# Kernel optimization log

Hardware: AMD Instinct MI355X
Metric: run time of the kernel (lower is better)

The kernel has to match this reference:

```python
import math
import jax, jax.numpy as jnp
import numpy as np

D = 256       # d_model
R = 64        # low-rank bottleneck
E = 3         # num experts
KS = (1, 3, 5)
EPS = 0.1     # sinkhorn epsilon
ITERS = 10    # sinkhorn iterations


def _ln(x, g, b):
    m = jnp.mean(x, -1, keepdims=True)
    v = jnp.mean((x - m) ** 2, -1, keepdims=True)
    return (x - m) * jax.lax.rsqrt(v + 1e-5) * g + b


def _gelu(x):
    return jax.nn.gelu(x, approximate=False)  # torch nn.GELU default (erf)


def setup_inputs() -> dict:
    key = jax.random.key(0)
    ks = jax.random.split(key, 12)
    s = 0.02
    B, Lt, La = 16, 1024, 2048
    return {
        "text_feat": jax.random.normal(ks[0], (B, Lt, D), jnp.float32),
        "audio_feat": jax.random.normal(ks[1], (B, La, D), jnp.float32),
        # shared OT projection (LayerNorm + Linear, shared across modalities)
        "ln_g": jnp.ones((D,), jnp.float32),
        "ln_b": jnp.zeros((D,), jnp.float32),
        "W_sh": jax.random.normal(ks[2], (D, D), jnp.float32) * s,
        "b_sh": jnp.zeros((D,), jnp.float32),
        # contradiction router: Linear(d+1->d) GELU Linear(d->E)
        "Wr1": jax.random.normal(ks[3], (D, D + 1), jnp.float32) * s,
        "br1": jnp.zeros((D,), jnp.float32),
        "Wr2": jax.random.normal(ks[4], (E, D), jnp.float32) * s,
        "br2": jnp.zeros((E,), jnp.float32),
        # 3 low-rank conv experts (stacked where shapes match)
        "down_W": jax.random.normal(ks[5], (E, R, D), jnp.float32) * s,
        "down_b": jnp.zeros((E, R), jnp.float32),
        "conv_w1": jax.random.normal(ks[6], (R, R, 1), jnp.float32) * s,
        "conv_w3": jax.random.normal(ks[7], (R, R, 3), jnp.float32) * s,
        "conv_w5": jax.random.normal(ks[8], (R, R, 5), jnp.float32) * s,
        "conv_b": jnp.zeros((E, R), jnp.float32),
        "up_W": jax.random.normal(ks[9], (E, D, R), jnp.float32) * s,
        "up_b": jnp.zeros((E, D), jnp.float32),
        "en_g": jnp.ones((E, D), jnp.float32),
        "en_b": jnp.zeros((E, D), jnp.float32),
    }


def reference(text_feat, audio_feat, ln_g, ln_b, W_sh, b_sh, Wr1, br1, Wr2, br2,
              down_W, down_b, conv_w1, conv_w3, conv_w5, conv_b, up_W, up_b, en_g, en_b):
    B, Lt, _ = text_feat.shape
    La = audio_feat.shape[1]

    # ---- shared projection (dropout = identity at eval) ----
    Tp = _ln(text_feat, ln_g, ln_b) @ W_sh.T + b_sh      # [B,Lt,D]
    Ap = _ln(audio_feat, ln_g, ln_b) @ W_sh.T + b_sh     # [B,La,D]

    # ---- cosine cost ----
    Tn = Tp / jnp.maximum(jnp.linalg.norm(Tp, axis=-1, keepdims=True), 1e-12)
    An = Ap / jnp.maximum(jnp.linalg.norm(Ap, axis=-1, keepdims=True), 1e-12)
    cost = 1.0 - jnp.einsum('bmd,bnd->bmn', Tn, An)      # [B,Lt,La]

    # ---- log-domain Sinkhorn (uniform marginals, no masks) ----
    log_K = -cost / (EPS + 1e-8)
    log_mu = jnp.full((B, Lt), -math.log(Lt), jnp.float32)
    log_nu = jnp.full((B, La), -math.log(La), jnp.float32)
    lu = jnp.zeros((B, Lt), jnp.float32)
    lv = jnp.zeros((B, La), jnp.float32)
    for _ in range(ITERS):
        lu = log_mu - jax.scipy.special.logsumexp(log_K + lv[:, None, :], axis=-1)
        lu = jnp.nan_to_num(jnp.clip(lu, -1e9, 1e9), nan=0.0, posinf=1e9, neginf=-1e9)
        lv = log_nu - jax.scipy.special.logsumexp(log_K + lu[:, :, None], axis=1)
        lv = jnp.nan_to_num(jnp.clip(lv, -1e9, 1e9), nan=0.0, posinf=1e9, neginf=-1e9)
    pi = jnp.exp(lu[:, :, None] + log_K + lv[:, None, :])
    pi = jnp.nan_to_num(pi, nan=0.0, posinf=1.0, neginf=0.0)  # [B,Lt,La]

    A_al = jnp.einsum('bmn,bnd->bmd', pi, Ap)            # [B,Lt,D]
    S = jnp.sum(Tp * A_al, -1)                           # [B,Lt]
    resid = jnp.abs(Tp - A_al)                           # [B,Lt,D]

    # ---- contradiction router ----
    rin = jnp.concatenate([S[..., None], resid], -1)     # [B,Lt,D+1]
    G = jax.nn.softmax(_gelu(rin @ Wr1.T + br1) @ Wr2.T + br2, axis=-1)  # [B,Lt,E]

    # ---- multi-scale low-rank conv MoE over contradiction residual ----
    convs = (conv_w1, conv_w3, conv_w5)
    x = resid
    out = jnp.zeros_like(Tp)
    for e in range(E):
        h = _gelu(x @ down_W[e].T + down_b[e])           # [B,Lt,R]
        k = convs[e].shape[-1]
        pad = (k - 1) // 2
        hc = jax.lax.conv_general_dilated(
            h.transpose(0, 2, 1), convs[e], (1,), [(pad, pad)],
            dimension_numbers=('NCH', 'OIH', 'NCH')) + conv_b[e][None, :, None]
        h = _gelu(hc).transpose(0, 2, 1)                 # [B,Lt,R]
        h = h @ up_W[e].T + up_b[e]                      # [B,Lt,D]
        eo = _ln(h + x, en_g[e], en_b[e])
        out = out + G[..., e:e + 1] * eo
    return out
```

## Files before the change

kernel.cpp:

```cpp
#include <hip/hip_runtime.h>
#include <cstdio>

#define D_ 256
#define LT 1024
#define LA 2048
#define NB 16
#define RR_ 64
#define NRT (NB*LT)
#define NRA (NB*LA)

#define DECQ  (-0.080645161f)
#define DECQ2 (-0.11634637f)

typedef short bf16x8 __attribute__((ext_vector_type(8)));
typedef float f32x4 __attribute__((ext_vector_type(4)));

__device__ __forceinline__ float gelu_f(float x) {
    return 0.5f * x * (1.0f + erff(x * 0.70710678118654752f));
}
__device__ __forceinline__ unsigned short f2bf(float f) {
    union { float f; unsigned int i; } c; c.f = f;
    unsigned int x = c.i;
    return (unsigned short)((x + 0x7fffu + ((x >> 16) & 1u)) >> 16);
}
__device__ __forceinline__ float exp2_fast(float x) {
#if __has_builtin(__builtin_amdgcn_exp2f)
    return __builtin_amdgcn_exp2f(x);
#else
    float r; asm("v_exp_f32 %0, %1" : "=v"(r) : "v"(x)); return r;
#endif
}
__device__ __forceinline__ unsigned int cvt_pk_bf16(float lo, float hi) {
    unsigned int r;
    asm("v_cvt_pk_bf16_f32 %0, %1, %2" : "=v"(r) : "v"(lo), "v"(hi));
    return r;
}

__global__ __launch_bounds__(256) void k_prep_all(
    const float* __restrict__ W_sh, const float* __restrict__ down_W,
    const float* __restrict__ up_W, const float* __restrict__ Wr1,
    unsigned short* __restrict__ Wb, unsigned short* __restrict__ dWb,
    unsigned short* __restrict__ uWb, unsigned short* __restrict__ Wr1b)
{
    int i = blockIdx.x * 256 + threadIdx.x;
    if (i < 65536) Wb[i] = f2bf(W_sh[i]);
    else if (i < 114688) { int j = i - 65536; dWb[j] = f2bf(down_W[j]); }
    else if (i < 163840) { int j = i - 114688; uWb[j] = f2bf(up_W[j]); }
    else { int j = i - 163840; int n = j >> 8, k = j & 255; Wr1b[j] = f2bf(Wr1[(long)n * 257 + 1 + k]); }
}

__global__ __launch_bounds__(256) void k_lnproj_mfma(
    const float* __restrict__ X, const float* __restrict__ g, const float* __restrict__ bln,
    const unsigned short* __restrict__ Wb, const float* __restrict__ bsh,
    float* __restrict__ Pf, unsigned short* __restrict__ Nb)
{
    __shared__ short xb[64][264];
    __shared__ short Bs[256][40];
    int tid = threadIdx.x;
    long row0 = (long)blockIdx.x * 64;
    {
        int lane = tid & 31, rg = tid >> 5;
        float4 ga = *(const float4*)(g + lane * 8);
        float4 gb2 = *(const float4*)(g + lane * 8 + 4);
        float4 ba = *(const float4*)(bln + lane * 8);
        float4 bb2 = *(const float4*)(bln + lane * 8 + 4);
        for (int it = 0; it < 8; it++) {
            int r = it * 8 + rg;
            const float4* xp4 = (const float4*)(X + (row0 + r) * D_);
            float4 a = xp4[lane * 2], b = xp4[lane * 2 + 1];
            float s = a.x + a.y + a.z + a.w + b.x + b.y + b.z + b.w;
#pragma unroll
            for (int off = 16; off >= 1; off >>= 1) s += __shfl_xor(s, off);
            float mean = s * (1.0f / 256.0f);
            float q = (a.x - mean) * (a.x - mean) + (a.y - mean) * (a.y - mean)
                    + (a.z - mean) * (a.z - mean) + (a.w - mean) * (a.w - mean)
                    + (b.x - mean) * (b.x - mean) + (b.y - mean) * (b.y - mean)
                    + (b.z - mean) * (b.z - mean) + (b.w - mean) * (b.w - mean);
#pragma unroll
            for (int off = 16; off >= 1; off >>= 1) q += __shfl_xor(q, off);
            float ivar = rsqrtf(q * (1.0f / 256.0f) + 1e-5f);
            unsigned int u0 = f2bf((a.x - mean) * ivar * ga.x + ba.x);
            unsigned int u1 = f2bf((a.y - mean) * ivar * ga.y + ba.y);
            unsigned int u2 = f2bf((a.z - mean) * ivar * ga.z + ba.z);
            unsigned int u3 = f2bf((a.w - mean) * ivar * ga.w + ba.w);
            unsigned int u4 = f2bf((b.x - mean) * ivar * gb2.x + bb2.x);
            unsigned int u5 = f2bf((b.y - mean) * ivar * gb2.y + bb2.y);
            unsigned int u6 = f2bf((b.z - mean) * ivar * gb2.z + bb2.z);
            unsigned int u7 = f2bf((b.w - mean) * ivar * gb2.w + bb2.w);
            int4 pv;
            pv.x = (int)(u0 | (u1 << 16)); pv.y = (int)(u2 | (u3 << 16));
            pv.z = (int)(u4 | (u5 << 16)); pv.w = (int)(u6 | (u7 << 16));
            *(int4*)&xb[r][lane * 8] = pv;
        }
    }
    __syncthreads();
    int wid = tid >> 6, lane = tid & 63;
    int l15 = lane & 15, kq = lane >> 4;
    int m_local = wid * 16;
    f32x4 acc[16];
#pragma unroll
    for (int j = 0; j < 16; j++) acc[j] = (f32x4){0.f, 0.f, 0.f, 0.f};
    for (int kt = 0; kt < 8; kt++) {
        int k0 = kt * 32;
#pragma unroll
        for (int h = 0; h < 4; h++) {
            int idx = tid + 256 * h;
            int n = idx >> 2, qc = idx & 3;
            *(int4*)&Bs[n][qc * 8] = *(const int4*)(Wb + (long)n * D_ + k0 + qc * 8);
        }
        __syncthreads();
        bf16x8 af = *(const bf16x8*)&xb[m_local + l15][k0 + kq * 8];
#pragma unroll
        for (int j = 0; j < 16; j++) {
            bf16x8 bf = *(const bf16x8*)&Bs[j * 16 + l15][kq * 8];
            acc[j] = __builtin_amdgcn_mfma_f32_16x16x32_bf16(af, bf, acc[j], 0, 0, 0);
        }
        __syncthreads();
    }
#pragma unroll
    for (int j = 0; j < 16; j++) {
        float bv = bsh[j * 16 + l15];
#pragma unroll
        for (int r = 0; r < 4; r++) acc[j][r] += bv;
    }
    float sq[4] = {0.f, 0.f, 0.f, 0.f};
#pragma unroll
    for (int j = 0; j < 16; j++)
#pragma unroll
        for (int r = 0; r < 4; r++) sq[r] += acc[j][r] * acc[j][r];
#pragma unroll
    for (int off = 8; off >= 1; off >>= 1) {
#pragma unroll
        for (int r = 0; r < 4; r++) sq[r] += __shfl_xor(sq[r], off);
    }
    float rinv[4];
#pragma unroll
    for (int r = 0; r < 4; r++) rinv[r] = 1.0f / fmaxf(sqrtf(sq[r]), 1e-12f);
#pragma unroll
    for (int j = 0; j < 16; j++) {
        int col = j * 16 + l15;
#pragma unroll
        for (int r = 0; r < 4; r++) {
            long m = row0 + m_local + kq * 4 + r;
            if (Pf) Pf[m * D_ + col] = acc[j][r];
            Nb[m * D_ + col] = f2bf(acc[j][r] * rinv[r]);
        }
    }
}

__global__ __launch_bounds__(256) void k_transpose_bf(
    const unsigned short* __restrict__ Anb, unsigned short* __restrict__ ApbT)
{
    __shared__ short t[64][68];
    int b = blockIdx.x;
    int n0 = blockIdx.y * 64;
    int d0 = blockIdx.z * 64;
    int tid = threadIdx.x;
#pragma unroll
    for (int h = 0; h < 2; h++) {
        int c = tid + 256 * h;
        int nr = c >> 3, ch = c & 7;
        *(int4*)&t[nr][ch * 8] = *(const int4*)(Anb + ((long)b * LA + n0 + nr) * D_ + d0 + ch * 8);
    }
    __syncthreads();
#pragma unroll
    for (int h = 0; h < 2; h++) {
        int c = tid + 256 * h;
        int d = c >> 3, nch = c & 7;
        unsigned short v[8];
#pragma unroll
        for (int k = 0; k < 8; k++) v[k] = (unsigned short)t[nch * 8 + k][d];
        int4 ov;
        ov.x = (int)((unsigned int)v[0] | ((unsigned int)v[1] << 16));
        ov.y = (int)((unsigned int)v[2] | ((unsigned int)v[3] << 16));
        ov.z = (int)((unsigned int)v[4] | ((unsigned int)v[5] << 16));
        ov.w = (int)((unsigned int)v[6] | ((unsigned int)v[7] << 16));
        *(int4*)(ApbT + ((long)b * D_ + d0 + d) * LA + n0 + nch * 8) = ov;
    }
}

__global__ __launch_bounds__(256) void k_cost_mfma(
    const unsigned short* __restrict__ Tnb, const unsigned short* __restrict__ Anb,
    unsigned char* __restrict__ logK8, unsigned char* __restrict__ logK8T)
{
    __shared__ short sm[2][128][48];
    short (*As)[48] = sm[0];
    short (*Bs)[48] = sm[1];
    unsigned char* tile = (unsigned char*)sm;
    int b = blockIdx.x;
    int m_blk = blockIdx.y * 128, n_blk = blockIdx.z * 128;
    int tid = threadIdx.x;
    int wid = tid >> 6, lane = tid & 63;
    int l15 = lane & 15, kq = lane >> 4;
    int wm0 = (wid >> 1) * 64, wn0 = (wid & 1) * 64;
    const unsigned short* Ab = Tnb + ((long)b * LT + m_blk) * D_;
    const unsigned short* Bb = Anb + ((long)b * LA + n_blk) * D_;
    f32x4 acc[4][4];
#pragma unroll
    for (int i = 0; i < 4; i++)
#pragma unroll
        for (int j = 0; j < 4; j++) acc[i][j] = (f32x4){0.f, 0.f, 0.f, 0.f};
    for (int kt = 0; kt < 8; kt++) {
        int k0 = kt * 32;
#pragma unroll
        for (int h = 0; h < 2; h++) {
            int idx = tid + 256 * h;
            int row = idx >> 2, ch = idx & 3;
            *(int4*)&As[row][ch * 8] = *(const int4*)(Ab + (long)row * D_ + k0 + ch * 8);
            *(int4*)&Bs[row][ch * 8] = *(const int4*)(Bb + (long)row * D_ + k0 + ch * 8);
        }
        __syncthreads();
        bf16x8 af[4], bfv[4];
#pragma unroll
        for (int i = 0; i < 4; i++) af[i] = *(const bf16x8*)&As[wm0 + i * 16 + l15][kq * 8];
#pragma unroll
        for (int j = 0; j < 4; j++) bfv[j] = *(const bf16x8*)&Bs[wn0 + j * 16 + l15][kq * 8];
#pragma unroll
        for (int i = 0; i < 4; i++)
#pragma unroll
            for (int j = 0; j < 4; j++)
                acc[i][j] = __builtin_amdgcn_mfma_f32_16x16x32_bf16(af[i], bfv[j], acc[i][j], 0, 0, 0);
        __syncthreads();
    }
#pragma unroll
    for (int i = 0; i < 4; i++) {
#pragma unroll
        for (int j = 0; j < 4; j++) {
            int n = wn0 + j * 16 + l15;
            long base = ((long)b * LT + m_blk + wm0 + i * 16 + kq * 4) * (long)LA + n_blk + n;
            unsigned int pk = 0;
#pragma unroll
            for (int r = 0; r < 4; r++) {
                float q = rintf((1.0f - acc[i][j][r]) * 124.0f);
                q = fminf(fmaxf(q, 0.0f), 255.0f);
                unsigned int qb = (unsigned int)q;
                pk |= qb << (8 * r);
                logK8[base + (long)r * LA] = (unsigned char)qb;
            }
            *(unsigned int*)&tile[n * 144 + wm0 + i * 16 + kq * 4] = pk;
        }
    }
    __syncthreads();
#pragma unroll
    for (int h = 0; h < 4; h++) {
        int idx = tid + 256 * h;
        int row = idx >> 3, ch = idx & 7;
        int4 v = *(const int4*)&tile[row * 144 + ch * 16];
        *(int4*)(logK8T + ((long)b * LA + n_blk + row) * (long)LT + m_blk + ch * 16) = v;
    }
}

__global__ __launch_bounds__(256) void k_rowlse2(
    const unsigned char* __restrict__ logK8, const float* __restrict__ lv2,
    float* __restrict__ lu2, int first)
{
    __shared__ float red[8][4];
    int b = blockIdx.x & 15;
    int mseg = blockIdx.x >> 4;
    int tid = threadIdx.x;
    int wid = tid >> 6, lane = tid & 63;
    float lvv[8] = {0.f, 0.f, 0.f, 0.f, 0.f, 0.f, 0.f, 0.f};
    if (!first) {
        const float* lvp = lv2 + (long)b * LA + tid * 8;
        float4 l0 = *(const float4*)lvp, l1 = *(const float4*)(lvp + 4);
        lvv[0] = l0.x; lvv[1] = l0.y; lvv[2] = l0.z; lvv[3] = l0.w;
        lvv[4] = l1.x; lvv[5] = l1.y; lvv[6] = l1.z; lvv[7] = l1.w;
    }
    const unsigned char* p = logK8 + ((long)b * LT + mseg * 8) * (long)LA + tid * 8;
#pragma unroll
    for (int r = 0; r < 8; r++) {
        uint2 w = *(const uint2*)(p + (long)r * LA);
        unsigned int w0 = w.x, w1 = w.y;
        float s = 0.f;
        s += exp2_fast(fmaf((float)(w0 & 0xffu),         DECQ2, lvv[0]));
        s += exp2_fast(fmaf((float)((w0 >> 8) & 0xffu),  DECQ2, lvv[1]));
        s += exp2_fast(fmaf((float)((w0 >> 16) & 0xffu), DECQ2, lvv[2]));
        s += exp2_fast(fmaf((float)(w0 >> 24),           DECQ2, lvv[3]));
        s += exp2_fast(fmaf((float)(w1 & 0xffu),         DECQ2, lvv[4]));
        s += exp2_fast(fmaf((float)((w1 >> 8) & 0xffu),  DECQ2, lvv[5]));
        s += exp2_fast(fmaf((float)((w1 >> 16) & 0xffu), DECQ2, lvv[6]));
        s += exp2_fast(fmaf((float)(w1 >> 24),           DECQ2, lvv[7]));
#pragma unroll
        for (int off = 32; off >= 1; off >>= 1) s += __shfl_xor(s, off);
        if (lane == 0) red[r][wid] = s;
    }
    __syncthreads();
    if (tid < 8) {
        float s = red[tid][0] + red[tid][1] + red[tid][2] + red[tid][3];
        lu2[(long)b * LT + mseg * 8 + tid] = -10.0f - __log2f(s);
    }
}

__global__ __launch_bounds__(256) void k_collse2(
    const unsigned char* __restrict__ logK8T, const float* __restrict__ lu2,
    float* __restrict__ lv2, int final_)
{
    __shared__ float red[16][2];
    int b = blockIdx.x & 15;
    int nseg = blockIdx.x >> 4;
    int tid = threadIdx.x;
    int t7 = tid & 127;
    int g = tid >> 7;
    int wid = tid >> 6, lane = tid & 63;
    const float* lup = lu2 + (long)b * LT + t7 * 8;
    float4 l0 = *(const float4*)lup, l1 = *(const float4*)(lup + 4);
    float lus[8] = {l0.x, l0.y, l0.z, l0.w, l1.x, l1.y, l1.z, l1.w};
    const unsigned char* base = logK8T + ((long)b * LA + nseg * 16) * (long)LT + t7 * 8;
#pragma unroll
    for (int it = 0; it < 8; it++) {
        int c = it * 2 + g;
        uint2 w = *(const uint2*)(base + (long)c * LT);
        unsigned int w0 = w.x, w1 = w.y;
        float s = 0.f;
        s += exp2_fast(fmaf((float)(w0 & 0xffu),         DECQ2, lus[0]));
        s += exp2_fast(fmaf((float)((w0 >> 8) & 0xffu),  DECQ2, lus[1]));
        s += exp2_fast(fmaf((float)((w0 >> 16) & 0xffu), DECQ2, lus[2]));
        s += exp2_fast(fmaf((float)(w0 >> 24),           DECQ2, lus[3]));
        s += exp2_fast(fmaf((float)(w1 & 0xffu),         DECQ2, lus[4]));
        s += exp2_fast(fmaf((float)((w1 >> 8) & 0xffu),  DECQ2, lus[5]));
        s += exp2_fast(fmaf((float)((w1 >> 16) & 0xffu), DECQ2, lus[6]));
        s += exp2_fast(fmaf((float)(w1 >> 24),           DECQ2, lus[7]));
#pragma unroll
        for (int off = 32; off >= 1; off >>= 1) s += __shfl_xor(s, off);
        if (lane == 0) red[c][wid & 1] = s;
    }
    __syncthreads();
    if (tid < 16) {
        float s = red[tid][0] + red[tid][1];
        lv2[(long)b * LA + nseg * 16 + tid] = final_ ? (0.00048828125f / s)
                                                     : (-11.0f - __log2f(s));
    }
}

__global__ __launch_bounds__(256) void k_scale_ev(
    unsigned short* __restrict__ ApbT, const float* __restrict__ ev)
{
    int b = blockIdx.x;
    int d = blockIdx.y;
    int tid = threadIdx.x;
    long off = ((long)b * D_ + d) * (long)LA + tid * 8;
    int4 v = *(const int4*)(ApbT + off);
    const float* ep = ev + (long)b * LA + tid * 8;
    float4 e0 = *(const float4*)ep, e1 = *(const float4*)(ep + 4);
    unsigned int u[4] = {(unsigned int)v.x, (unsigned int)v.y, (unsigned int)v.z, (unsigned int)v.w};
    float ee[8] = {e0.x, e0.y, e0.z, e0.w, e1.x, e1.y, e1.z, e1.w};
    unsigned int o[4];
#pragma unroll
    for (int k = 0; k < 4; k++) {
        float lo = __uint_as_float(u[k] << 16) * ee[2 * k];
        float hi = __uint_as_float(u[k] & 0xffff0000u) * ee[2 * k + 1];
        o[k] = cvt_pk_bf16(lo, hi);
    }
    int4 ov; ov.x = (int)o[0]; ov.y = (int)o[1]; ov.z = (int)o[2]; ov.w = (int)o[3];
    *(int4*)(ApbT + off) = ov;
}

__global__ __launch_bounds__(256) void k_pi2(
    const unsigned char* __restrict__ logK8, const unsigned short* __restrict__ Av,
    const float* __restrict__ lu2, float* __restrict__ Apart)
{
    __shared__ short As[32][48];
    __shared__ short Bs[256][48];
    __shared__ float eus[32];
    int b = blockIdx.x;
    int kh = blockIdx.y;
    int m_blk = blockIdx.z * 32;
    int nbase = kh * 1024;
    int tid = threadIdx.x;
    if (tid < 32) eus[tid] = exp2_fast(lu2[(long)b * LT + m_blk + tid]);
    int wid = tid >> 6, lane = tid & 63;
    int l15 = lane & 15, kq = lane >> 4;
    int wm0 = (wid & 1) * 16, wd0 = (wid >> 1) * 128;
    f32x4 acc[8];
#pragma unroll
    for (int j = 0; j < 8; j++) acc[j] = (f32x4){0.f, 0.f, 0.f, 0.f};
    const unsigned char* Kbase = logK8 + ((long)b * LT + m_blk) * (long)LA + nbase;
    const unsigned short* Bbase = Av + (long)b * D_ * (long)LA + nbase;
    int arow = tid >> 3, ac4 = (tid & 7) * 4;
    for (int kt = 0; kt < 32; kt++) {
        int n0 = kt * 32;
        {
            unsigned int w = *(const unsigned int*)(Kbase + (long)arow * LA + n0 + ac4);
            float e0 = exp2_fast((float)(w & 0xffu) * DECQ2);
            float e1 = exp2_fast((float)((w >> 8) & 0xffu) * DECQ2);
            float e2 = exp2_fast((float)((w >> 16) & 0xffu) * DECQ2);
            float e3 = exp2_fast((float)(w >> 24) * DECQ2);
            uint2 pv;
            pv.x = cvt_pk_bf16(e0, e1);
            pv.y = cvt_pk_bf16(e2, e3);
            *(uint2*)&As[arow][ac4] = pv;
        }
#pragma unroll
        for (int h = 0; h < 4; h++) {
            int idx = tid + 256 * h;
            int row = idx >> 2, ch = idx & 3;
            *(int4*)&Bs[row][ch * 8] = *(const int4*)(Bbase + (long)row * LA + n0 + ch * 8);
        }
        __syncthreads();
        bf16x8 af = *(const bf16x8*)&As[wm0 + l15][kq * 8];
        bf16x8 bfv[8];
#pragma unroll
        for (int j = 0; j < 8; j++) bfv[j] = *(const bf16x8*)&Bs[wd0 + j * 16 + l15][kq * 8];
#pragma unroll
        for (int j = 0; j < 8; j++)
            acc[j] = __builtin_amdgcn_mfma_f32_16x16x32_bf16(af, bfv[j], acc[j], 0, 0, 0);
        __syncthreads();
    }
    float* dst = Apart + (long)kh * (NB * (long)LT * D_);
#pragma unroll
    for (int r = 0; r < 4; r++) {
        int rloc = wm0 + kq * 4 + r;
        float eu = eus[rloc];
        long obase = ((long)b * LT + m_blk + rloc) * D_;
#pragma unroll
        for (int j = 0; j < 8; j++)
            dst[obase + wd0 + j * 16 + l15] = acc[j][r] * eu;
    }
}

__global__ __launch_bounds__(256) void k_sresid(
    const float* __restrict__ Tp, const float* __restrict__ Apart,
    float* __restrict__ resid, unsigned short* __restrict__ residb, float* __restrict__ S)
{
    __shared__ float red[4];
    int b = blockIdx.x & 15;
    int m = blockIdx.x >> 4;
    long row = (long)b * LT + m;
    int tid = threadIdx.x;
    long idx = row * D_ + tid;
    float t = Tp[idx];
    float a = Apart[idx] + Apart[idx + (long)NB * LT * D_];
    float rr = fabsf(t - a);
    resid[idx] = rr;
    residb[idx] = f2bf(rr);
    float p = t * a;
#pragma unroll
    for (int off = 32; off >= 1; off >>= 1) p += __shfl_xor(p, off);
    if ((tid & 63) == 0) red[tid >> 6] = p;
    __syncthreads();
    if (tid == 0) S[row] = red[0] + red[1] + red[2] + red[3];
}

__global__ __launch_bounds__(256) void k_router_fused(
    const unsigned short* __restrict__ residb, const unsigned short* __restrict__ Wr1b,
    const float* __restrict__ Wr1, const float* __restrict__ br1,
    const float* __restrict__ S, const float* __restrict__ Wr2,
    const float* __restrict__ br2, float* __restrict__ G)
{
    __shared__ short xb[16][264];
    __shared__ short Bs[256][40];
    __shared__ float red[4][3][16];
    int tid = threadIdx.x;
    long row0 = (long)blockIdx.x * 16;
#pragma unroll
    for (int h = 0; h < 2; h++) {
        int idx = tid + 256 * h;
        int row = idx >> 5, ch = idx & 31;
        *(int4*)&xb[row][ch * 8] = *(const int4*)(residb + (row0 + row) * D_ + ch * 8);
    }
    __syncthreads();
    int wid = tid >> 6, lane = tid & 63;
    int l15 = lane & 15, kq = lane >> 4;
    f32x4 acc[4];
#pragma unroll
    for (int j = 0; j < 4; j++) acc[j] = (f32x4){0.f, 0.f, 0.f, 0.f};
    for (int kt = 0; kt < 8; kt++) {
        int k0 = kt * 32;
#pragma unroll
        for (int h = 0; h < 4; h++) {
            int idx = tid + 256 * h;
            int n = idx >> 2, qc = idx & 3;
            *(int4*)&Bs[n][qc * 8] = *(const int4*)(Wr1b + (long)n * D_ + k0 + qc * 8);
        }
        __syncthreads();
        bf16x8 af = *(const bf16x8*)&xb[l15][k0 + kq * 8];
#pragma unroll
        for (int j = 0; j < 4; j++) {
            bf16x8 bf = *(const bf16x8*)&Bs[wid * 64 + j * 16 + l15][kq * 8];
            acc[j] = __builtin_amdgcn_mfma_f32_16x16x32_bf16(af, bf, acc[j], 0, 0, 0);
        }
        __syncthreads();
    }
    float sv[4];
#pragma unroll
    for (int r = 0; r < 4; r++) sv[r] = S[row0 + kq * 4 + r];
    float le[3][4] = {};
#pragma unroll
    for (int j = 0; j < 4; j++) {
        int col = wid * 64 + j * 16 + l15;
        float w0 = Wr1[(long)col * 257];
        float bv = br1[col];
        float w2a = Wr2[col], w2b = Wr2[256 + col], w2c = Wr2[512 + col];
#pragma unroll
        for (int r = 0; r < 4; r++) {
            float hv = gelu_f(acc[j][r] + sv[r] * w0 + bv);
            le[0][r] += hv * w2a;
            le[1][r] += hv * w2b;
            le[2][r] += hv * w2c;
        }
    }
#pragma unroll
    for (int off = 8; off >= 1; off >>= 1)
#pragma unroll
        for (int e = 0; e < 3; e++)
#pragma unroll
            for (int r = 0; r < 4; r++) le[e][r] += __shfl_xor(le[e][r], off);
    if (l15 == 0) {
#pragma unroll
        for (int e = 0; e < 3; e++)
#pragma unroll
            for (int r = 0; r < 4; r++) red[wid][e][kq * 4 + r] = le[e][r];
    }
    __syncthreads();
    if (tid < 16) {
        float L0 = red[0][0][tid] + red[1][0][tid] + red[2][0][tid] + red[3][0][tid] + br2[0];
        float L1 = red[0][1][tid] + red[1][1][tid] + red[2][1][tid] + red[3][1][tid] + br2[1];
        float L2 = red[0][2][tid] + red[1][2][tid] + red[2][2][tid] + red[3][2][tid] + br2[2];
        float mx = fmaxf(L0, fmaxf(L1, L2));
        float e0 = __expf(L0 - mx), e1 = __expf(L1 - mx), e2 = __expf(L2 - mx);
        float inv = 1.0f / (e0 + e1 + e2);
        long m = row0 + tid;
        G[m] = e0 * inv; G[NRT + m] = e1 * inv; G[2 * NRT + m] = e2 * inv;
    }
}

__global__ __launch_bounds__(256) void k_down_mfma(
    const unsigned short* __restrict__ residb, const unsigned short* __restrict__ dWb,
    const float* __restrict__ db, float* __restrict__ hall)
{
    __shared__ short xb[64][264];
    __shared__ short Bs[64][40];
    int tid = threadIdx.x;
    int e = blockIdx.y;
    int b = blockIdx.x & 15;
    int mseg = blockIdx.x >> 4;
    long row0 = (long)b * LT + mseg * 64;
    const unsigned short* dWe = dWb + (long)e * RR_ * D_;
    float* h = hall + (long)e * NRT * RR_;
#pragma unroll
    for (int hh = 0; hh < 8; hh++) {
        int idx = tid + 256 * hh;
        int row = idx >> 5, ch = idx & 31;
        *(int4*)&xb[row][ch * 8] = *(const int4*)(residb + (row0 + row) * D_ + ch * 8);
    }
    __syncthreads();
    int wid = tid >> 6, lane = tid & 63;
    int l15 = lane & 15, kq = lane >> 4;
    int m_local = wid * 16;
    f32x4 acc[4];
#pragma unroll
    for (int j = 0; j < 4; j++) acc[j] = (f32x4){0.f, 0.f, 0.f, 0.f};
    for (int kt = 0; kt < 8; kt++) {
        int k0 = kt * 32;
        {
            int n = tid >> 2, qc = tid & 3;
            *(int4*)&Bs[n][qc * 8] = *(const int4*)(dWe + (long)n * D_ + k0 + qc * 8);
        }
        __syncthreads();
        bf16x8 af = *(const bf16x8*)&xb[m_local + l15][k0 + kq * 8];
#pragma unroll
        for (int j = 0; j < 4; j++) {
            bf16x8 bf = *(const bf16x8*)&Bs[j * 16 + l15][kq * 8];
            acc[j] = __builtin_amdgcn_mfma_f32_16x16x32_bf16(af, bf, acc[j], 0, 0, 0);
        }
        __syncthreads();
    }
#pragma unroll
    for (int j = 0; j < 4; j++) {
        int col = j * 16 + l15;
        float bv = db[e * RR_ + col];
#pragma unroll
        for (int r = 0; r < 4; r++) {
            long m = row0 + m_local + kq * 4 + r;
            h[m * RR_ + col] = gelu_f(acc[j][r] + bv);
        }
    }
}

__global__ __launch_bounds__(256) void k_conv_all(
    const float* __restrict__ hall, const float* __restrict__ cw1,
    const float* __restrict__ cw3, const float* __restrict__ cw5,
    const float* __restrict__ conv_b, unsigned short* __restrict__ hcbb)
{
    __shared__ float hs[68][68];
    __shared__ float wt[64][64];
    int e = blockIdx.y;
    const float* w = (e == 0) ? cw1 : ((e == 1) ? cw3 : cw5);
    int ksz = (e == 0) ? 1 : ((e == 1) ? 3 : 5);
    const float* h = hall + (long)e * NRT * RR_;
    unsigned short* hcb = hcbb + (long)e * NRT * RR_;
    const float* cb = conv_b + e * 64;
    int b = blockIdx.x & 15;
    int m0 = (blockIdx.x >> 4) * 64;
    int tid = threadIdx.x;
    int pad = (ksz - 1) >> 1;
    for (int idx = tid; idx < 68 * 16; idx += 256) {
        int mr = idx >> 4, i4 = idx & 15;
        int mm = m0 - 2 + mr;
        float4 vv = { 0.f, 0.f, 0.f, 0.f };
        if (mm >= 0 && mm < LT) vv = *(const float4*)(h + ((long)b * LT + mm) * RR_ + i4 * 4);
        *(float4*)&hs[mr][i4 * 4] = vv;
    }
    int tx = tid & 15, ty = tid >> 4;
    float acc[4][4] = {};
    for (int t = 0; t < ksz; t++) {
        __syncthreads();
        for (int idx = tid; idx < 4096; idx += 256) {
            int i = idx & 63, j = idx >> 6;
            wt[i][j] = w[(long)j * RR_ * ksz + i * ksz + t];
        }
        __syncthreads();
        int roff = ty * 4 + 2 + t - pad;
        for (int i4 = 0; i4 < 16; i4++) {
            float4 h0 = *(const float4*)&hs[roff + 0][i4 * 4];
            float4 h1 = *(const float4*)&hs[roff + 1][i4 * 4];
            float4 h2 = *(const float4*)&hs[roff + 2][i4 * 4];
            float4 h3 = *(const float4*)&hs[roff + 3][i4 * 4];
            float hh[4][4] = { { h0.x, h0.y, h0.z, h0.w }, { h1.x, h1.y, h1.z, h1.w },
                               { h2.x, h2.y, h2.z, h2.w }, { h3.x, h3.y, h3.z, h3.w } };
#pragma unroll
            for (int s = 0; s < 4; s++) {
                float4 wv = *(const float4*)&wt[i4 * 4 + s][tx * 4];
#pragma unroll
                for (int r = 0; r < 4; r++) {
                    acc[r][0] += hh[r][s] * wv.x;
                    acc[r][1] += hh[r][s] * wv.y;
                    acc[r][2] += hh[r][s] * wv.z;
                    acc[r][3] += hh[r][s] * wv.w;
                }
            }
        }
    }
    float4 bb = *(const float4*)(cb + tx * 4);
#pragma unroll
    for (int r = 0; r < 4; r++) {
        long m = (long)b * LT + m0 + ty * 4 + r;
        unsigned long long pv =
              (unsigned long long)f2bf(gelu_f(acc[r][0] + bb.x))
            | ((unsigned long long)f2bf(gelu_f(acc[r][1] + bb.y)) << 16)
            | ((unsigned long long)f2bf(gelu_f(acc[r][2] + bb.z)) << 32)
            | ((unsigned long long)f2bf(gelu_f(acc[r][3] + bb.w)) << 48);
        *(unsigned long long*)(hcb + m * RR_ + tx * 4) = pv;
    }
}

__global__ __launch_bounds__(256) void k_up3(
    const unsigned short* __restrict__ hcbb, const unsigned short* __restrict__ uWb,
    const float* __restrict__ up_b, const float* __restrict__ resid,
    const float* __restrict__ en_g, const float* __restrict__ en_b,
    const float* __restrict__ G, float* __restrict__ out)
{
    __shared__ short hs[64][88];
    __shared__ short Bs[256][40];
    int tid = threadIdx.x;
    int b = blockIdx.x & 15;
    int mseg = blockIdx.x >> 4;
    long row0 = (long)b * LT + mseg * 64;
    int wid = tid >> 6, lane = tid & 63;
    int l15 = lane & 15, kq = lane >> 4;
    int m_local = wid * 16;
    long mrow[4];
#pragma unroll
    for (int r = 0; r < 4; r++) mrow[r] = row0 + m_local + kq * 4 + r;
    f32x4 outacc[16];
#pragma unroll
    for (int j = 0; j < 16; j++) outacc[j] = (f32x4){0.f, 0.f, 0.f, 0.f};
    for (int e = 0; e < 3; e++) {
        __syncthreads();
        const unsigned short* hcb = hcbb + (long)e * NRT * RR_;
        const unsigned short* uWe = uWb + (long)e * 16384;
#pragma unroll
        for (int hh = 0; hh < 2; hh++) {
            int idx = tid + 256 * hh;
            int row = idx >> 3, ch = idx & 7;
            *(int4*)&hs[row][ch * 8] = *(const int4*)(hcb + (row0 + row) * RR_ + ch * 8);
        }
        f32x4 acc[16];
#pragma unroll
        for (int j = 0; j < 16; j++) acc[j] = (f32x4){0.f, 0.f, 0.f, 0.f};
        for (int kt = 0; kt < 2; kt++) {
            int k0 = kt * 32;
#pragma unroll
            for (int hh = 0; hh < 4; hh++) {
                int idx = tid + 256 * hh;
                int n = idx >> 2, qc = idx & 3;
                *(int4*)&Bs[n][qc * 8] = *(const int4*)(uWe + (long)n * RR_ + k0 + qc * 8);
            }
            __syncthreads();
            bf16x8 af = *(const bf16x8*)&hs[m_local + l15][k0 + kq * 8];
#pragma unroll
            for (int j = 0; j < 16; j++) {
                bf16x8 bf = *(const bf16x8*)&Bs[j * 16 + l15][kq * 8];
                acc[j] = __builtin_amdgcn_mfma_f32_16x16x32_bf16(af, bf, acc[j], 0, 0, 0);
            }
            __syncthreads();
        }
        const float* ub = up_b + e * 256;
#pragma unroll
        for (int j = 0; j < 16; j++) {
            int col = j * 16 + l15;
            float bv = ub[col];
#pragma unroll
            for (int r = 0; r < 4; r++)
                acc[j][r] += bv + resid[mrow[r] * D_ + col];
        }
        float s[4] = {0.f, 0.f, 0.f, 0.f};
#pragma unroll
        for (int j = 0; j < 16; j++)
#pragma unroll
            for (int r = 0; r < 4; r++) s[r] += acc[j][r];
#pragma unroll
        for (int off = 8; off >= 1; off >>= 1)
#pragma unroll
            for (int r = 0; r < 4; r++) s[r] += __shfl_xor(s[r], off);
        float mn[4];
#pragma unroll
        for (int r = 0; r < 4; r++) mn[r] = s[r] * (1.0f / 256.0f);
        float q[4] = {0.f, 0.f, 0.f, 0.f};
#pragma unroll
        for (int j = 0; j < 16; j++)
#pragma unroll
            for (int r = 0; r < 4; r++) { float d = acc[j][r] - mn[r]; q[r] += d * d; }
#pragma unroll
        for (int off = 8; off >= 1; off >>= 1)
#pragma unroll
            for (int r = 0; r < 4; r++) q[r] += __shfl_xor(q[r], off);
        float iv[4], gv[4];
#pragma unroll
        for (int r = 0; r < 4; r++) {
            iv[r] = rsqrtf(q[r] * (1.0f / 256.0f) + 1e-5f);
            gv[r] = G[(long)e * NRT + mrow[r]];
        }
        const float* eg = en_g + e * 256;
        const float* eb = en_b + e * 256;
#pragma unroll
        for (int j = 0; j < 16; j++) {
            int col = j * 16 + l15;
            float egc = eg[col], ebc = eb[col];
#pragma unroll
            for (int r = 0; r < 4; r++)
                outacc[j][r] += gv[r] * ((acc[j][r] - mn[r]) * iv[r] * egc + ebc);
        }
    }
#pragma unroll
    for (int j = 0; j < 16; j++) {
        int col = j * 16 + l15;
#pragma unroll
        for (int r = 0; r < 4; r++)
            out[mrow[r] * D_ + col] = outacc[j][r];
    }
}

extern "C" void kernel_launch(void* const* d_in, const int* in_sizes, int n_in,
                              void* d_out, int out_size, void* d_ws, size_t ws_size,
                              hipStream_t stream)
{
    const float* text   = (const float*)d_in[0];
    const float* audio  = (const float*)d_in[1];
    const float* ln_g   = (const float*)d_in[2];
    const float* ln_b   = (const float*)d_in[3];
    const float* W_sh   = (const float*)d_in[4];
    const float* b_sh   = (const float*)d_in[5];
    const float* Wr1    = (const float*)d_in[6];
    const float* br1    = (const float*)d_in[7];
    const float* Wr2    = (const float*)d_in[8];
    const float* br2    = (const float*)d_in[9];
    const float* down_W = (const float*)d_in[10];
    const float* down_b = (const float*)d_in[11];
    const float* cw1    = (const float*)d_in[12];
    const float* cw3    = (const float*)d_in[13];
    const float* cw5    = (const float*)d_in[14];
    const float* conv_b = (const float*)d_in[15];
    const float* up_W   = (const float*)d_in[16];
    const float* up_b   = (const float*)d_in[17];
    const float* en_g   = (const float*)d_in[18];
    const float* en_b   = (const float*)d_in[19];

    float* ws = (float*)d_ws;
    float*          Tp    = ws;
    unsigned short* Tnb   = (unsigned short*)(ws + 4194304);
    unsigned short* Anb   = (unsigned short*)(ws + 6291456);
    unsigned short* ApbT  = (unsigned short*)(ws + 10485760);
    unsigned char*  logK8 = (unsigned char*)(ws + 14680064);
    float*          Apart = ws + 23068672;
    float*          resid = ws + 31457280;
    unsigned short* residb= (unsigned short*)(ws + 35651584);
    float*          lu2   = ws + 37748736;
    float*          lv2   = ws + 37765120;
    float*          Sb    = ws + 37797888;
    float*          Gb    = ws + 37814272;
    unsigned short* Wb    = (unsigned short*)(ws + 37863424);
    unsigned short* dWb   = (unsigned short*)(ws + 37896192);
    unsigned short* uWb   = (unsigned short*)(ws + 37920768);
    unsigned short* Wr1b  = (unsigned short*)(ws + 37945344);
    size_t need_bytes = (size_t)37978112 * 4;
    if (ws_size < need_bytes) {
        fprintf(stderr, "kernel_launch: ws_size %zu < needed %zu\n", ws_size, need_bytes);
        return;
    }
    float*          hall = ws + 14680064;
    unsigned short* hcbb = (unsigned short*)(ws + 17825792);
    unsigned char*  logK8T = (unsigned char*)(ws + 23068672);

    k_prep_all<<<896, 256, 0, stream>>>(W_sh, down_W, up_W, Wr1, Wb, dWb, uWb, Wr1b);
    k_lnproj_mfma<<<NRT / 64, 256, 0, stream>>>(text, ln_g, ln_b, Wb, b_sh, Tp, Tnb);
    k_lnproj_mfma<<<NRA / 64, 256, 0, stream>>>(audio, ln_g, ln_b, Wb, b_sh, nullptr, Anb);
    k_transpose_bf<<<dim3(NB, LA / 64, D_ / 64), 256, 0, stream>>>(Anb, ApbT);
    k_cost_mfma<<<dim3(NB, LT / 128, LA / 128), 256, 0, stream>>>(Tnb, Anb, logK8, logK8T);
    for (int it = 0; it < 10; it++) {
        k_rowlse2<<<NRT / 8, 256, 0, stream>>>(logK8, lv2, lu2, it == 0 ? 1 : 0);
        k_collse2<<<NB * (LA / 16), 256, 0, stream>>>(logK8T, lu2, lv2, it == 9 ? 1 : 0);
    }
    k_scale_ev<<<dim3(NB, D_), 256, 0, stream>>>(ApbT, lv2);
    k_pi2<<<dim3(NB, 2, LT / 32), 256, 0, stream>>>(logK8, ApbT, lu2, Apart);
    k_sresid<<<NRT, 256, 0, stream>>>(Tp, Apart, resid, residb, Sb);
    k_router_fused<<<NRT / 16, 256, 0, stream>>>(residb, Wr1b, Wr1, br1, Sb, Wr2, br2, Gb);
    k_down_mfma<<<dim3(NRT / 64, 3), 256, 0, stream>>>(residb, dWb, down_b, hall);
    k_conv_all<<<dim3(NRT / 64, 3), 256, 0, stream>>>(hall, cw1, cw3, cw5, conv_b, hcbb);
    k_up3<<<NRT / 64, 256, 0, stream>>>(hcbb, uWb, up_b, resid, en_g, en_b, Gb, (float*)d_out);
}
```

Before: 533.7 us.

## Build A fragments in registers and prefetch B tiles in k_pi2

```diff
diff --git a/kernel.cpp b/kernel.cpp
--- a/kernel.cpp
+++ b/kernel.cpp
@@ -359,8 +359,7 @@
     const unsigned char* __restrict__ logK8, const unsigned short* __restrict__ Av,
     const float* __restrict__ lu2, float* __restrict__ Apart)
 {
-    __shared__ short As[32][48];
-    __shared__ short Bs[256][48];
+    __shared__ short Bs[256][40];
     __shared__ float eus[32];
     int b = blockIdx.x;
     int kh = blockIdx.y;
@@ -374,37 +373,47 @@
     f32x4 acc[8];
 #pragma unroll
     for (int j = 0; j < 8; j++) acc[j] = (f32x4){0.f, 0.f, 0.f, 0.f};
-    const unsigned char* Kbase = logK8 + ((long)b * LT + m_blk) * (long)LA + nbase;
-    const unsigned short* Bbase = Av + (long)b * D_ * (long)LA + nbase;
-    int arow = tid >> 3, ac4 = (tid & 7) * 4;
+    const unsigned char* Arow = logK8 + ((long)b * LT + m_blk + wm0 + l15) * (long)LA + nbase + kq * 8;
+    const unsigned short* Bptr = Av + (long)b * D_ * (long)LA + nbase
+                               + (long)(tid >> 2) * LA + (tid & 3) * 8;
+    int brow = tid >> 2, bch = (tid & 3) * 8;
+    int4 rb0 = *(const int4*)(Bptr);
+    int4 rb1 = *(const int4*)(Bptr + 64 * LA);
+    int4 rb2 = *(const int4*)(Bptr + 128 * LA);
+    int4 rb3 = *(const int4*)(Bptr + 192 * LA);
     for (int kt = 0; kt < 32; kt++) {
         int n0 = kt * 32;
-        {
-            unsigned int w = *(const unsigned int*)(Kbase + (long)arow * LA + n0 + ac4);
-            float e0 = exp2_fast((float)(w & 0xffu) * DECQ2);
-            float e1 = exp2_fast((float)((w >> 8) & 0xffu) * DECQ2);
-            float e2 = exp2_fast((float)((w >> 16) & 0xffu) * DECQ2);
-            float e3 = exp2_fast((float)(w >> 24) * DECQ2);
-            uint2 pv;
-            pv.x = cvt_pk_bf16(e0, e1);
-            pv.y = cvt_pk_bf16(e2, e3);
-            *(uint2*)&As[arow][ac4] = pv;
-        }
-#pragma unroll
-        for (int h = 0; h < 4; h++) {
-            int idx = tid + 256 * h;
-            int row = idx >> 2, ch = idx & 3;
-            *(int4*)&Bs[row][ch * 8] = *(const int4*)(Bbase + (long)row * LA + n0 + ch * 8);
-        }
-        __syncthreads();
-        bf16x8 af = *(const bf16x8*)&As[wm0 + l15][kq * 8];
-        bf16x8 bfv[8];
-#pragma unroll
-        for (int j = 0; j < 8; j++) bfv[j] = *(const bf16x8*)&Bs[wd0 + j * 16 + l15][kq * 8];
-#pragma unroll
-        for (int j = 0; j < 8; j++)
-            acc[j] = __builtin_amdgcn_mfma_f32_16x16x32_bf16(af, bfv[j], acc[j], 0, 0, 0);
-        __syncthreads();
+        uint2 w = *(const uint2*)(Arow + n0);
+        unsigned int w0 = w.x, w1 = w.y;
+        float e0 = exp2_fast((float)(w0 & 0xffu) * DECQ2);
+        float e1 = exp2_fast((float)((w0 >> 8) & 0xffu) * DECQ2);
+        float e2 = exp2_fast((float)((w0 >> 16) & 0xffu) * DECQ2);
+        float e3 = exp2_fast((float)(w0 >> 24) * DECQ2);
+        float e4 = exp2_fast((float)(w1 & 0xffu) * DECQ2);
+        float e5 = exp2_fast((float)((w1 >> 8) & 0xffu) * DECQ2);
+        float e6 = exp2_fast((float)((w1 >> 16) & 0xffu) * DECQ2);
+        float e7 = exp2_fast((float)(w1 >> 24) * DECQ2);
+        union { unsigned int u[4]; bf16x8 v; } A;
+        A.u[0] = cvt_pk_bf16(e0, e1); A.u[1] = cvt_pk_bf16(e2, e3);
+        A.u[2] = cvt_pk_bf16(e4, e5); A.u[3] = cvt_pk_bf16(e6, e7);
+        bf16x8 af = A.v;
+        __syncthreads();
+        *(int4*)&Bs[brow][bch]       = rb0;
+        *(int4*)&Bs[brow + 64][bch]  = rb1;
+        *(int4*)&Bs[brow + 128][bch] = rb2;
+        *(int4*)&Bs[brow + 192][bch] = rb3;
+        if (kt < 31) {
+            rb0 = *(const int4*)(Bptr + n0 + 32);
+            rb1 = *(const int4*)(Bptr + 64 * LA + n0 + 32);
+            rb2 = *(const int4*)(Bptr + 128 * LA + n0 + 32);
+            rb3 = *(const int4*)(Bptr + 192 * LA + n0 + 32);
+        }
+        __syncthreads();
+#pragma unroll
+        for (int j = 0; j < 8; j++) {
+            bf16x8 bfv = *(const bf16x8*)&Bs[wd0 + j * 16 + l15][kq * 8];
+            acc[j] = __builtin_amdgcn_mfma_f32_16x16x32_bf16(af, bfv, acc[j], 0, 0, 0);
+        }
     }
     float* dst = Apart + (long)kh * (NB * (long)LT * D_);
 #pragma unroll
```

Result: no change. 542.9 us (+1.7%).
